# Kernel tuning notes

Measured on AMD Instinct MI355X. Metric: run time of the kernel, lower is better.

Reference implementation:

```python
import jax, jax.numpy as jnp
import numpy as np

B, N, D = 64, 256, 64          # datasets, samples per dataset, feature dim per variable (indim/2)
H, H2, OUT = 128, 64, 3        # hdlayers, hdlayers//2, outdim
REG, SIGMA, ALPHA = 1.0, 1.0, 2
BN_EPS = 1e-5


def _linear(k, fan_in, fan_out):
    kw, kb = jax.random.split(k)
    lim = 1.0 / np.sqrt(fan_in)
    w = jax.random.uniform(kw, (fan_in, fan_out), jnp.float32, -lim, lim)
    b = jax.random.uniform(kb, (fan_out,), jnp.float32, -lim, lim)
    return w, b


def setup_inputs() -> dict:
    key = jax.random.key(0)
    ks = jax.random.split(key, 10)
    w11_1, b11_1 = _linear(ks[2], D, H2)
    w11_2, b11_2 = _linear(ks[3], H2, H2)
    w12_1, b12_1 = _linear(ks[4], 2 * H2, H)
    w12_2, b12_2 = _linear(ks[5], H, H2)
    wc1, bc1 = _linear(ks[6], H2, OUT)
    w2, b2 = _linear(ks[7], OUT + 2, H2)
    wc2, bc2 = _linear(ks[8], H2, OUT)
    return {
        'x': jax.random.normal(ks[0], (B, N, D), jnp.float32),
        'y': jax.random.normal(ks[1], (B, N, D), jnp.float32),
        'w11_1': w11_1, 'b11_1': b11_1, 'w11_2': w11_2, 'b11_2': b11_2,
        'w12_1': w12_1, 'b12_1': b12_1, 'w12_2': w12_2, 'b12_2': b12_2,
        'wc1': wc1, 'bc1': bc1,
        'bn_gamma': jnp.ones((OUT + 2,), jnp.float32),
        'bn_beta': jnp.zeros((OUT + 2,), jnp.float32),
        'w2': w2, 'b2': b2, 'wc2': wc2, 'bc2': bc2,
    }


def _fro_normalize(t):
    # divide each [N, D] slice by its Frobenius norm
    return t / jnp.linalg.norm(t, axis=(1, 2), keepdims=True)


def _linear_regressor(x, y, reg):
    b, n, d = x.shape
    X = jnp.concatenate([jnp.ones((b, n, 1), x.dtype), x], axis=2)  # [B,N,d+1]
    P1 = jnp.einsum('bni,bnj->bij', X, X)                           # X^T X
    ridge = reg * jnp.eye(d + 1, dtype=x.dtype).at[0, 0].set(0.0)   # G^T G
    P2 = jnp.linalg.inv(P1 + ridge[None])
    P4 = X @ (P2 @ (jnp.swapaxes(X, 1, 2) @ y))
    loss = jnp.sum((y - P4) ** 2, axis=(1, 2))
    return loss, P4


def _gauss_kernel(x):
    # x: [B, N, F] -> [B, N, N]
    xn = jnp.sum(x * x, axis=-1)
    dist = xn[:, :, None] + xn[:, None, :] - 2.0 * jnp.einsum('bnd,bmd->bnm', x, x)
    return jnp.exp(-dist / SIGMA)


def _renyi_from_kernel(k):
    tr = jnp.trace(k, axis1=1, axis2=2)
    k = k / tr[:, None, None]
    ev = jnp.abs(jnp.linalg.eigvalsh(k))          # batched symeig eigenvalues
    return (1.0 / (1 - ALPHA)) * jnp.log2(jnp.sum(ev ** ALPHA, axis=-1))


def _renyi_mi(a, b):
    # batched normalized Renyi mutual information, a/b: [B, N, F]
    ka, kb = _gauss_kernel(a), _gauss_kernel(b)
    Hx = _renyi_from_kernel(ka)
    Hy = _renyi_from_kernel(kb)
    Hxy = _renyi_from_kernel(ka * kb)
    return (Hx + Hy - Hxy) / jnp.maximum(Hx, Hy)


def reference(x, y, w11_1, b11_1, w11_2, b11_2, w12_1, b12_1, w12_2, b12_2,
              wc1, bc1, bn_gamma, bn_beta, w2, b2, wc2, bc2):
    mlp11 = lambda t: jnp.maximum(t @ w11_1 + b11_1, 0.0) @ w11_2 + b11_2
    out_x = mlp11(x)                                  # [B,N,H2]
    out_y = mlp11(y)

    out_c = jnp.concatenate([out_x, out_y], axis=2)   # [B,N,2*H2]
    out_c = jnp.maximum(out_c @ w12_1 + b12_1, 0.0)
    out_c = jnp.maximum(out_c @ w12_2 + b12_2, 0.0)
    out_c = out_c.mean(axis=1)                        # [B,H2]
    out_c = out_c @ wc1 + bc1                         # [B,OUT]
    prob1 = jax.nn.softmax(out_c, axis=1)

    out_xn = _fro_normalize(out_x)
    out_yn = _fro_normalize(out_y)
    xx = _fro_normalize(x)
    yy = _fro_normalize(y)

    rx, px = _linear_regressor(out_xn, yy, REG)       # predict y from f(x)
    ry, py = _linear_regressor(out_yn, xx, REG)       # predict x from f(y)

    ex = _renyi_mi(yy - px, x)                        # [B]
    ey = _renyi_mi(xx - py, y)

    rxy = jnp.stack([ex, ey], axis=1)                 # [B,2]
    in_c = jnp.concatenate([out_c, rxy], axis=1)      # [B,OUT+2]
    mu = in_c.mean(axis=0)
    var = in_c.var(axis=0)                            # biased, as in torch BN training
    in_c = (in_c - mu) / jnp.sqrt(var + BN_EPS) * bn_gamma + bn_beta
    in_c = jnp.maximum(in_c @ w2 + b2, 0.0)
    out_c_f = in_c @ wc2 + bc2
    prob2 = jax.nn.softmax(out_c_f, axis=1)

    return (out_c, rx, ry, ex, ey, out_c_f, prob1, prob2)
```

## Files before the change

kernel.cpp:

```cpp
#include <hip/hip_runtime.h>
#include <math.h>

#define NB 64
#define NS 256
#define ND 64
#define NH2 64
#define NH 128
#define WSTRIDE 4224


#define F4E(v_, e_) ((e_)==0?(v_).x:((e_)==1?(v_).y:((e_)==2?(v_).z:(v_).w)))

typedef __attribute__((ext_vector_type(8))) short bf16x8;
typedef __attribute__((ext_vector_type(4))) float f32x4;

__device__ __forceinline__ unsigned short f2bf(float f){
    union { float f; unsigned int u; } v; v.f = f;
    unsigned int r = v.u + 0x7fffu + ((v.u >> 16) & 1u);
    return (unsigned short)(r >> 16);
}
__device__ __forceinline__ float bf2f(unsigned short h){
    union { unsigned int u; float f; } v; v.u = ((unsigned int)h) << 16;
    return v.f;
}
__device__ __forceinline__ void sw2(unsigned short* ph, unsigned short* pl, int idx, float f){
    unsigned short h = f2bf(f);
    ph[idx] = h;
    pl[idx] = f2bf(f - bf2f(h));
}
__device__ __forceinline__ void sw2x2(unsigned short* ph, unsigned short* pl, int idx, float f0, float f1){
    unsigned short h0 = f2bf(f0), h1 = f2bf(f1);
    ushort2 hh; hh.x = h0; hh.y = h1;
    *(ushort2*)(ph + idx) = hh;
    ushort2 ll; ll.x = f2bf(f0 - bf2f(h0)); ll.y = f2bf(f1 - bf2f(h1));
    *(ushort2*)(pl + idx) = ll;
}

#define LD8(P_, row_, kb_) (*(const bf16x8*)((const char*)(P_) + (size_t)(row_)*144 + (kb_)))

__device__ __forceinline__ f32x4 mm64(
    const unsigned short* Ah, const unsigned short* Al,
    const unsigned short* Bh, const unsigned short* Bl,
    int ar, int br, int lrow, int lkb, f32x4 acc)
{
    const int ra = ar + lrow, rb = br + lrow;
    bf16x8 ah0 = LD8(Ah, ra, lkb), ah1 = LD8(Ah, ra, lkb+64);
    bf16x8 al0 = LD8(Al, ra, lkb), al1 = LD8(Al, ra, lkb+64);
    bf16x8 bh0 = LD8(Bh, rb, lkb), bh1 = LD8(Bh, rb, lkb+64);
    bf16x8 bl0 = LD8(Bl, rb, lkb), bl1 = LD8(Bl, rb, lkb+64);
    acc = __builtin_amdgcn_mfma_f32_16x16x32_bf16(ah0, bh0, acc, 0,0,0);
    acc = __builtin_amdgcn_mfma_f32_16x16x32_bf16(ah1, bh1, acc, 0,0,0);
    acc = __builtin_amdgcn_mfma_f32_16x16x32_bf16(ah0, bl0, acc, 0,0,0);
    acc = __builtin_amdgcn_mfma_f32_16x16x32_bf16(ah1, bl1, acc, 0,0,0);
    acc = __builtin_amdgcn_mfma_f32_16x16x32_bf16(al0, bh0, acc, 0,0,0);
    acc = __builtin_amdgcn_mfma_f32_16x16x32_bf16(al1, bh1, acc, 0,0,0);
    return acc;
}

__global__ __launch_bounds__(512) void k1_fused(
    const float* __restrict__ x, const float* __restrict__ y,
    const float* __restrict__ w11_1, const float* __restrict__ b11_1,
    const float* __restrict__ w11_2, const float* __restrict__ b11_2,
    const float* __restrict__ w12_1, const float* __restrict__ b12_1,
    const float* __restrict__ w12_2, const float* __restrict__ b12_2,
    float* __restrict__ out_x, float* __restrict__ out_y,
    float* __restrict__ mean_part)
{
    const int b = blockIdx.x >> 2, tile = blockIdx.x & 3;
    const int t = threadIdx.x;
    const int lane = t & 63, wv = t >> 6;
    const int lrow = lane & 15;
    const int lkb  = (lane >> 4) * 16;
    const int row0g = b*NS + tile*64;

    __shared__ unsigned short XYh[9216], XYl[9216];
    __shared__ unsigned short W1h[4608], W1l[4608];
    __shared__ unsigned short W2h[4608], W2l[4608];
    __shared__ unsigned short Hh [9216], Hl [9216];
    __shared__ unsigned short Oh [9216], Ol [9216];
    __shared__ float msum[8*68];

    #pragma unroll
    for (int u=0;u<4;u++){
        int id = t + 512*u;
        int r = id>>4, c0 = (id&15)*4;
        const float* src = (r < 64) ? (x + ((size_t)(row0g + r))*ND)
                                    : (y + ((size_t)(row0g + r - 64))*ND);
        float4 v = *(const float4*)(src + c0);
        sw2x2(XYh, XYl, r*72 + c0,   v.x, v.y);
        sw2x2(XYh, XYl, r*72 + c0+2, v.z, v.w);
    }
    {
        int rp = t>>4, c0 = (t&15)*4;
        float4 a0 = *(const float4*)(w11_1 + (size_t)(2*rp  )*64 + c0);
        float4 a1 = *(const float4*)(w11_1 + (size_t)(2*rp+1)*64 + c0);
        float4 b0 = *(const float4*)(w11_2 + (size_t)(2*rp  )*64 + c0);
        float4 b1 = *(const float4*)(w11_2 + (size_t)(2*rp+1)*64 + c0);
        #pragma unroll
        for (int i2=0;i2<4;i2++){
            sw2x2(W1h, W1l, (c0+i2)*72 + 2*rp, F4E(a0,i2), F4E(a1,i2));
            sw2x2(W2h, W2l, (c0+i2)*72 + 2*rp, F4E(b0,i2), F4E(b1,i2));
        }
    }
    __syncthreads();

    {
        const int ar = 16*wv;
        #pragma unroll
        for (int jt=0; jt<4; jt++){
            float bb = b11_1[jt*16 + lrow];
            f32x4 acc = {bb,bb,bb,bb};
            acc = mm64(XYh, XYl, W1h, W1l, ar, jt*16, lrow, lkb, acc);
            #pragma unroll
            for (int e=0;e<4;e++){
                int row = ar + (lane>>4)*4 + e;
                int col = jt*16 + lrow;
                sw2(Hh, Hl, row*72 + col, fmaxf(acc[e], 0.f));
            }
        }
    }
    __syncthreads();

    #pragma unroll
    for (int u=0;u<2;u++){
        int id = t + 512*u;
        int krp = id>>5, c0 = (id&31)*4;
        float4 v0 = *(const float4*)(w12_1 + (size_t)(2*krp  )*NH + c0);
        float4 v1 = *(const float4*)(w12_1 + (size_t)(2*krp+1)*NH + c0);
        #pragma unroll
        for (int i2=0;i2<4;i2++)
            sw2x2(XYh, XYl, (c0+i2)*72 + 2*krp, F4E(v0,i2), F4E(v1,i2));
    }
    {
        const int ar = 16*wv;
        #pragma unroll
        for (int jt=0; jt<4; jt++){
            float bb = b11_2[jt*16 + lrow];
            f32x4 acc = {bb,bb,bb,bb};
            acc = mm64(Hh, Hl, W2h, W2l, ar, jt*16, lrow, lkb, acc);
            #pragma unroll
            for (int e=0;e<4;e++){
                int row = ar + (lane>>4)*4 + e;
                int col = jt*16 + lrow;
                float v = acc[e];
                sw2(Oh, Ol, row*72 + col, v);
                float* dst = (row < 64) ? out_x : out_y;
                dst[((size_t)(row0g + (row & 63)))*NH2 + col] = v;
            }
        }
    }
    __syncthreads();

    const int rt = wv & 3, cq = wv >> 2;
    f32x4 acc3[4];
    #pragma unroll
    for (int q=0; q<4; q++){
        float bb = b12_1[(4*cq+q)*16 + lrow];
        f32x4 v = {bb,bb,bb,bb};
        acc3[q] = v;
    }
    #pragma unroll
    for (int q=0; q<4; q++)
        acc3[q] = mm64(Oh, Ol, XYh, XYl, 16*rt, 16*(4*cq+q), lrow, lkb, acc3[q]);
    __syncthreads();

    #pragma unroll
    for (int u=0;u<2;u++){
        int id = t + 512*u;
        int krp = id>>5, c0 = (id&31)*4;
        float4 v0 = *(const float4*)(w12_1 + (size_t)(64+2*krp  )*NH + c0);
        float4 v1 = *(const float4*)(w12_1 + (size_t)(64+2*krp+1)*NH + c0);
        #pragma unroll
        for (int i2=0;i2<4;i2++)
            sw2x2(XYh, XYl, (c0+i2)*72 + 2*krp, F4E(v0,i2), F4E(v1,i2));
    }
    {
        int krp = t>>4, c0 = (t&15)*4;
        float4 h0a = *(const float4*)(w12_2 + (size_t)(2*krp  )*NH2 + c0);
        float4 h0b = *(const float4*)(w12_2 + (size_t)(2*krp+1)*NH2 + c0);
        float4 h1a = *(const float4*)(w12_2 + (size_t)(64+2*krp  )*NH2 + c0);
        float4 h1b = *(const float4*)(w12_2 + (size_t)(64+2*krp+1)*NH2 + c0);
        #pragma unroll
        for (int i2=0;i2<4;i2++){
            sw2x2(W2h, W2l, (c0+i2)*72 + 2*krp, F4E(h0a,i2), F4E(h0b,i2));
            sw2x2(W1h, W1l, (c0+i2)*72 + 2*krp, F4E(h1a,i2), F4E(h1b,i2));
        }
    }
    __syncthreads();

    #pragma unroll
    for (int q=0; q<4; q++)
        acc3[q] = mm64(Oh, Ol, XYh, XYl, 64 + 16*rt, 16*(4*cq+q), lrow, lkb, acc3[q]);
    #pragma unroll
    for (int q=0; q<4; q++){
        #pragma unroll
        for (int e=0;e<4;e++){
            int row = 16*rt + (lane>>4)*4 + e;
            int col = 16*(4*cq+q) + lrow;
            float v = fmaxf(acc3[q][e], 0.f);
            int idx = (col < 64) ? (row*72 + col) : ((64+row)*72 + (col-64));
            sw2(Hh, Hl, idx, v);
        }
    }
    __syncthreads();

    {
        f32x4 acc2[2];
        #pragma unroll
        for (int q=0; q<2; q++){
            const int jc = 2*cq + q;
            float bb = b12_2[jc*16 + lrow];
            f32x4 v = {bb,bb,bb,bb};
            acc2[q] = v;
            acc2[q] = mm64(Hh, Hl, W2h, W2l, 16*rt,      16*jc, lrow, lkb, acc2[q]);
            acc2[q] = mm64(Hh, Hl, W1h, W1l, 64 + 16*rt, 16*jc, lrow, lkb, acc2[q]);
        }
        #pragma unroll
        for (int q=0; q<2; q++){
            const int jc = 2*cq + q;
            float s = fmaxf(acc2[q][0],0.f) + fmaxf(acc2[q][1],0.f)
                    + fmaxf(acc2[q][2],0.f) + fmaxf(acc2[q][3],0.f);
            s += __shfl_down(s, 32);
            s += __shfl_down(s, 16);
            if (lane < 16) msum[wv*68 + jc*16 + lane] = s;
        }
    }
    __syncthreads();
    if (t < 64){
        const int w0 = (t>>5)*4;
        float ss = msum[(w0+0)*68 + t] + msum[(w0+1)*68 + t]
                 + msum[(w0+2)*68 + t] + msum[(w0+3)*68 + t];
        mean_part[((size_t)(b*4+tile))*64 + t] = ss;
    }
}

__global__ __launch_bounds__(256) void k2ab(
    const float* __restrict__ fx, const float* __restrict__ fy,
    const float* __restrict__ x, const float* __restrict__ y,
    float* __restrict__ wbuf)
{
    const int bs = blockIdx.x;
    const int side = bs & 1, b = bs >> 1;
    const float* feat = side ? fy : fx;
    const float* targ = side ? x : y;
    float* wb = wbuf + (size_t)bs*WSTRIDE;
    const int t = threadIdx.x;
    const int lane = t & 63, wv = t >> 6;
    const int lrow = lane & 15;
    const int lkb  = (lane >> 4) * 16;
    const float inv256 = 1.0f/256.0f;

    __shared__ float Wf[64*68];
    __shared__ float Rf[64*68];
    __shared__ unsigned short Zh[4608], Zl[4608], Th[4608], Tl[4608];
    __shared__ unsigned short Eh[4608], El[4608];
    __shared__ unsigned short Wth[2][4608], Wtl[2][4608];
    __shared__ float cspA[16*68], cspB[16*68];
    __shared__ float szs[64], sts[64];
    __shared__ float sc[8], red4[4];

    {
        float szp0=0.f,szp1=0.f,szp2=0.f,szp3=0.f;
        float stp0=0.f,stp1=0.f,stp2=0.f,stp3=0.f;
        float tsq=0.f;
        for (int c=0;c<4;c++){
            #pragma unroll
            for (int u=0;u<4;u++){
                int id = t + 256*u;
                int r = id>>4, c0 = (id&15)*4;
                float4 v = *(const float4*)(feat + ((size_t)(b*NS + c*64 + r))*NH2 + c0);
                float4 w = *(const float4*)(targ + ((size_t)(b*NS + c*64 + r))*ND + c0);
                szp0+=v.x; szp1+=v.y; szp2+=v.z; szp3+=v.w;
                stp0+=w.x; stp1+=w.y; stp2+=w.z; stp3+=w.w;
                tsq += w.x*w.x + w.y*w.y + w.z*w.z + w.w*w.w;
            }
        }
        const int g2 = t>>4, c0 = (t&15)*4;
        cspA[g2*68 + c0+0] = szp0; cspA[g2*68 + c0+1] = szp1;
        cspA[g2*68 + c0+2] = szp2; cspA[g2*68 + c0+3] = szp3;
        cspB[g2*68 + c0+0] = stp0; cspB[g2*68 + c0+1] = stp1;
        cspB[g2*68 + c0+2] = stp2; cspB[g2*68 + c0+3] = stp3;
        float tq = tsq;
        #pragma unroll
        for (int off=32; off; off>>=1) tq += __shfl_down(tq, off);
        if (lane==0) red4[wv] = tq;
    }
    __syncthreads();
    if (t < 64){
        float sa=0.f, sb=0.f;
        #pragma unroll
        for (int g2=0; g2<16; g2++){ sa += cspA[g2*68+t]; sb += cspB[g2*68+t]; }
        szs[t] = sa; sts[t] = sb;
        float s2 = sa*sa;
        #pragma unroll
        for (int off=32; off; off>>=1) s2 += __shfl_down(s2, off);
        if (t==0) sc[2] = s2;
    }
    if (t==0) sc[1] = red4[0]+red4[1]+red4[2]+red4[3];
    __syncthreads();

    f32x4 accA[4], accR[4];
    #pragma unroll
    for (int jt=0;jt<4;jt++){
        f32x4 z = {0.f,0.f,0.f,0.f};
        accA[jt]=z; accR[jt]=z;
    }
    for (int c=0;c<4;c++){
        if (c) __syncthreads();
        #pragma unroll
        for (int u=0;u<4;u++){
            int id = t + 256*u;
            int r = id>>4, c0 = (id&15)*4;
            float4 v = *(const float4*)(feat + ((size_t)(b*NS + c*64 + r))*NH2 + c0);
            float4 w = *(const float4*)(targ + ((size_t)(b*NS + c*64 + r))*ND + c0);
            v.x -= szs[c0+0]*inv256; v.y -= szs[c0+1]*inv256;
            v.z -= szs[c0+2]*inv256; v.w -= szs[c0+3]*inv256;
            sw2(Zh,Zl,(c0+0)*72+r, v.x); sw2(Zh,Zl,(c0+1)*72+r, v.y);
            sw2(Zh,Zl,(c0+2)*72+r, v.z); sw2(Zh,Zl,(c0+3)*72+r, v.w);
            sw2(Th,Tl,(c0+0)*72+r, w.x); sw2(Th,Tl,(c0+1)*72+r, w.y);
            sw2(Th,Tl,(c0+2)*72+r, w.z); sw2(Th,Tl,(c0+3)*72+r, w.w);
        }
        __syncthreads();
        #pragma unroll
        for (int jt=0;jt<4;jt++){
            accA[jt] = mm64(Zh,Zl,Zh,Zl, 16*wv, 16*jt, lrow, lkb, accA[jt]);
            accR[jt] = mm64(Zh,Zl,Th,Tl, 16*wv, 16*jt, lrow, lkb, accR[jt]);
        }
    }
    {
        const int gi0 = 16*wv + (lane>>4)*4;
        #pragma unroll
        for (int jt=0;jt<4;jt++){
            #pragma unroll
            for (int e=0;e<4;e++){
                Wf[(gi0+e)*68 + 16*jt + lrow] = accA[jt][e];
                Rf[(gi0+e)*68 + 16*jt + lrow] = accR[jt][e];
            }
        }
    }
    __syncthreads();
    if (t<64){
        float dg = Wf[t*68+t];
        #pragma unroll
        for (int off=32; off; off>>=1) dg += __shfl_down(dg, off);
        if (t==0){
            float zn2 = dg + sc[2]*inv256;
            sc[0] = 1.0f/sqrtf(zn2);
            sc[1] = 1.0f/sqrtf(sc[1]);
        }
    }
    __syncthreads();
    const float zinv = sc[0], tinv = sc[1];
    const float z2 = zinv*zinv, zt = zinv*tinv;
    const float i23 = 2.0f/3.0f, i13 = 1.0f/3.0f;
    const int i = t>>2, qd = t&3;
    {
        #pragma unroll
        for (int q=0;q<4;q++){
            const int j = qd*16 + q*4;
            float4 a4 = *(const float4*)(Wf + i*68 + j);
            float e0 = i23*z2*a4.x - ((i==j  ) ? i13 : 0.f);
            float e1 = i23*z2*a4.y - ((i==j+1) ? i13 : 0.f);
            float e2 = i23*z2*a4.z - ((i==j+2) ? i13 : 0.f);
            float e3 = i23*z2*a4.w - ((i==j+3) ? i13 : 0.f);
            sw2x2(Eh, El, i*72 + j,   e0, e1);
            sw2x2(Eh, El, i*72 + j+2, e2, e3);
            float4 rv = *(float4*)(Rf + i*68 + j);
            float r0 = i23*zt*rv.x;
            float r1 = i23*zt*rv.y;
            float r2 = i23*zt*rv.z;
            float r3 = i23*zt*rv.w;
            *(float4*)(Rf + i*68 + j) = make_float4(r0,r1,r2,r3);
            sw2(Wth[0], Wtl[0], (j  )*72 + i, r0);
            sw2(Wth[0], Wtl[0], (j+1)*72 + i, r1);
            sw2(Wth[0], Wtl[0], (j+2)*72 + i, r2);
            sw2(Wth[0], Wtl[0], (j+3)*72 + i, r3);
        }
    }
    __syncthreads();

    int cur = 0;
    for (int n=0; n<12; n++){
        f32x4 acc[4];
        #pragma unroll
        for (int jt=0; jt<4; jt++){
            f32x4 zz = {0.f,0.f,0.f,0.f};
            acc[jt] = mm64(Eh, El, Wth[cur], Wtl[cur], 16*wv, jt*16, lrow, lkb, zz);
        }
        const int gi0 = 16*wv + (lane>>4)*4;
        #pragma unroll
        for (int jt=0; jt<4; jt++){
            const int gj = jt*16 + lrow;
            float w0 = Rf[(gi0  )*68 + gj] - acc[jt][0];
            float w1 = Rf[(gi0+1)*68 + gj] - acc[jt][1];
            float w2 = Rf[(gi0+2)*68 + gj] - acc[jt][2];
            float w3 = Rf[(gi0+3)*68 + gj] - acc[jt][3];
            sw2x2(Wth[cur^1], Wtl[cur^1], gj*72 + gi0,   w0, w1);
            sw2x2(Wth[cur^1], Wtl[cur^1], gj*72 + gi0+2, w2, w3);
            if (n == 11){
                Wf[(gi0  )*68 + gj] = w0;  wb[(gi0  )*64 + gj] = w0;
                Wf[(gi0+1)*68 + gj] = w1;  wb[(gi0+1)*64 + gj] = w1;
                Wf[(gi0+2)*68 + gj] = w2;  wb[(gi0+2)*64 + gj] = w2;
                Wf[(gi0+3)*68 + gj] = w3;  wb[(gi0+3)*64 + gj] = w3;
            }
        }
        cur ^= 1;
        __syncthreads();
    }

    if (t < 64){
        float s = 0.f;
        for (int i2=0; i2<64; i2++) s += szs[i2]*Wf[i2*68 + t];
        wb[4096+t] = (tinv*sts[t] - zinv*s) * inv256;
    }
    if (t==0){ wb[4160] = zinv; wb[4161] = tinv; }
}

__global__ __launch_bounds__(256) void kRG(
    const float* __restrict__ fx, const float* __restrict__ fy,
    const float* __restrict__ x, const float* __restrict__ y,
    const float* __restrict__ wbuf,
    float* __restrict__ part3, float* __restrict__ dout)
{
    const int blk = blockIdx.x;
    const int jh = blk & 1;
    const int b = (blk >> 1) & (NB-1);
    const int side = (blk >> 1) >> 6;
    const float* feat = side ? fy : fx;
    const float* targ = side ? x : y;
    const float* bmat = side ? y : x;
    const float* wb = wbuf + (size_t)(b*2+side)*WSTRIDE;
    const int t = threadIdx.x;
    const int lane = t & 63, wv = t >> 6;
    const int lrow = lane & 15, lkb = (lane>>4)*16;

    __shared__ unsigned short resA[256*72];
    __shared__ unsigned short tgB [256*72];
    __shared__ unsigned short Zh[2*4608], Zl[2*4608];
    __shared__ unsigned short Wth[4608], Wtl[4608];
    __shared__ float c0s[64];
    __shared__ float nAs[256], nBs[256];
    __shared__ float red[4][3];
    __shared__ float lred[4];

    #pragma unroll
    for (int u=0;u<4;u++){
        int id = t + 256*u;
        int k = id>>4, c0 = (id&15)*4;
        float4 v = *(const float4*)(wb + (size_t)k*64 + c0);
        sw2(Wth, Wtl, (c0+0)*72 + k, v.x);
        sw2(Wth, Wtl, (c0+1)*72 + k, v.y);
        sw2(Wth, Wtl, (c0+2)*72 + k, v.z);
        sw2(Wth, Wtl, (c0+3)*72 + k, v.w);
    }
    if (t<64) c0s[t] = wb[4096+t];
    const float zinv = wb[4160], tinv = wb[4161];
    #pragma unroll
    for (int u=0;u<16;u++){
        int id = t + 256*u;
        int r = id>>4, c0 = (id&15)*4;
        float4 v = *(const float4*)(bmat + ((size_t)(b*NS+r))*ND + c0);
        ushort4 h;
        h.x=f2bf(v.x); h.y=f2bf(v.y); h.z=f2bf(v.z); h.w=f2bf(v.w);
        *(ushort4*)(tgB + r*72 + c0) = h;
    }
    #pragma unroll
    for (int u=0;u<4;u++){
        int id = t + 256*u;
        int r = id>>4, c0 = (id&15)*4;
        float4 v = *(const float4*)(feat + ((size_t)(b*NS + r))*NH2 + c0);
        sw2x2(Zh, Zl, r*72+c0,   v.x, v.y);
        sw2x2(Zh, Zl, r*72+c0+2, v.z, v.w);
    }
    __syncthreads();

    float lacc = 0.f;
    for (int c=0; c<4; c++){
        if (c < 3){
            unsigned short* zh = Zh + ((c+1)&1)*4608;
            unsigned short* zl = Zl + ((c+1)&1)*4608;
            #pragma unroll
            for (int u=0;u<4;u++){
                int id = t + 256*u;
                int r = id>>4, c0 = (id&15)*4;
                float4 v = *(const float4*)(feat + ((size_t)(b*NS + (c+1)*64 + r))*NH2 + c0);
                sw2x2(zh, zl, r*72+c0,   v.x, v.y);
                sw2x2(zh, zl, r*72+c0+2, v.z, v.w);
            }
        }
        const unsigned short* zh = Zh + (c&1)*4608;
        const unsigned short* zl = Zl + (c&1)*4608;
        f32x4 acc[4];
        #pragma unroll
        for (int jt=0; jt<4; jt++){
            f32x4 zz = {0.f,0.f,0.f,0.f};
            acc[jt] = mm64(zh, zl, Wth, Wtl, 16*wv, jt*16, lrow, lkb, zz);
        }
        const int r0 = 16*wv + (lane>>4)*4;
        #pragma unroll
        for (int jt=0; jt<4; jt++){
            const int gj = jt*16 + lrow;
            const float cc = c0s[gj];
            #pragma unroll
            for (int e=0;e<4;e++){
                const int grow = c*64 + r0 + e;
                float q = targ[((size_t)(b*NS+grow))*ND + gj];
                float rr = tinv*q - zinv*acc[jt][e] - cc;
                lacc += rr*rr;
                resA[grow*72 + gj] = f2bf(rr);
            }
        }
        __syncthreads();
    }

    {
        float l = lacc;
        #pragma unroll
        for (int off=32; off; off>>=1) l += __shfl_down(l, off);
        if (lane==0) lred[wv] = l;
    }
    {
        float sa=0.f, sb=0.f;
        #pragma unroll
        for (int j8=0;j8<8;j8++){
            bf16x8 va = *(const bf16x8*)((const char*)resA + (size_t)t*144 + j8*16);
            bf16x8 vb = *(const bf16x8*)((const char*)tgB  + (size_t)t*144 + j8*16);
            #pragma unroll
            for (int e2=0;e2<8;e2++){
                float fa = bf2f((unsigned short)va[e2]);
                float fb = bf2f((unsigned short)vb[e2]);
                sa += fa*fa; sb += fb*fb;
            }
        }
        nAs[t] = sa; nBs[t] = sb;
    }
    __syncthreads();
    if (t==0 && jh==0)
        dout[(side?256:192)+b] = lred[0]+lred[1]+lred[2]+lred[3];

    const char* pA = (const char*)resA;
    const char* pB = (const char*)tgB;
    const f32x4 zero4 = {0.f, 0.f, 0.f, 0.f};
    const float CEXP = -2.8853900817779268f;

    float Sa=0.f, Sb=0.f, Sab=0.f;
    #pragma unroll
    for (int it=0; it<4; it++){
        const int i0 = wv*64 + it*16;
        const int arow = i0 + lrow;
        bf16x8 aA0 = *(const bf16x8*)(pA + arow*144 + lkb);
        bf16x8 aA1 = *(const bf16x8*)(pA + arow*144 + lkb + 64);
        bf16x8 aB0 = *(const bf16x8*)(pB + arow*144 + lkb);
        bf16x8 aB1 = *(const bf16x8*)(pB + arow*144 + lkb + 64);
        float nAi[4], nBi[4];
        #pragma unroll
        for (int e=0;e<4;e++){
            int gi = i0 + (lane>>4)*4 + e;
            nAi[e] = nAs[gi]; nBi[e] = nBs[gi];
        }
        #pragma unroll
        for (int jt=0; jt<8; jt++){
            const int j0 = jh*128 + jt*16;
            const int brow = j0 + lrow;
            bf16x8 bA0 = *(const bf16x8*)(pA + brow*144 + lkb);
            bf16x8 bA1 = *(const bf16x8*)(pA + brow*144 + lkb + 64);
            bf16x8 bB0 = *(const bf16x8*)(pB + brow*144 + lkb);
            bf16x8 bB1 = *(const bf16x8*)(pB + brow*144 + lkb + 64);
            f32x4 cA = __builtin_amdgcn_mfma_f32_16x16x32_bf16(aA0, bA0, zero4, 0, 0, 0);
            cA = __builtin_amdgcn_mfma_f32_16x16x32_bf16(aA1, bA1, cA, 0, 0, 0);
            f32x4 cB = __builtin_amdgcn_mfma_f32_16x16x32_bf16(aB0, bB0, zero4, 0, 0, 0);
            cB = __builtin_amdgcn_mfma_f32_16x16x32_bf16(aB1, bB1, cB, 0, 0, 0);
            const int gj = j0 + lrow;
            const float nAj = nAs[gj], nBj = nBs[gj];
            #pragma unroll
            for (int e=0;e<4;e++){
                const int gi = i0 + (lane>>4)*4 + e;
                const float dda = (gi==gj) ? 0.f : (nAi[e] + nAj - 2.f*cA[e]);
                const float ddb = (gi==gj) ? 0.f : (nBi[e] + nBj - 2.f*cB[e]);
                const float ka2 = exp2f(CEXP*dda);
                const float kb2 = exp2f(CEXP*ddb);
                Sa += ka2; Sb += kb2; Sab += ka2*kb2;
            }
        }
    }
    #pragma unroll
    for (int off=32; off; off>>=1){
        Sa += __shfl_down(Sa,off); Sb += __shfl_down(Sb,off); Sab += __shfl_down(Sab,off);
    }
    if (lane==0){ red[wv][0]=Sa; red[wv][1]=Sb; red[wv][2]=Sab; }
    __syncthreads();
    if (t==0){
        float* o = part3 + (size_t)blk*3;
        o[0] = red[0][0]+red[1][0]+red[2][0]+red[3][0];
        o[1] = red[0][1]+red[1][1]+red[2][1]+red[3][1];
        o[2] = red[0][2]+red[1][2]+red[2][2]+red[3][2];
    }
}

__global__ __launch_bounds__(64) void k4_final(
    const float* __restrict__ mean_part, const float* __restrict__ part3,
    const float* __restrict__ wc1, const float* __restrict__ bc1,
    const float* __restrict__ bn_gamma, const float* __restrict__ bn_beta,
    const float* __restrict__ w2, const float* __restrict__ b2,
    const float* __restrict__ wc2, const float* __restrict__ bc2,
    float* __restrict__ dout)
{
    const int t = threadIdx.x;
    __shared__ float ic[64][5];
    __shared__ float mu[5], iv[5];

    float o0 = bc1[0], o1 = bc1[1], o2 = bc1[2];
    for (int c=0;c<64;c++){
        float mv = mean_part[(t*4+0)*64+c] + mean_part[(t*4+1)*64+c]
                 + mean_part[(t*4+2)*64+c] + mean_part[(t*4+3)*64+c];
        mv *= (1.0f/256.0f);
        o0 += mv*wc1[c*3+0]; o1 += mv*wc1[c*3+1]; o2 += mv*wc1[c*3+2];
    }
    dout[t*3+0]=o0; dout[t*3+1]=o1; dout[t*3+2]=o2;
    {
        float m = fmaxf(o0,fmaxf(o1,o2));
        float e0=__expf(o0-m), e1=__expf(o1-m), e2=__expf(o2-m);
        float inv = 1.f/(e0+e1+e2);
        dout[640+t*3+0]=e0*inv; dout[640+t*3+1]=e1*inv; dout[640+t*3+2]=e2*inv;
    }
    float exy[2];
    #pragma unroll
    for (int side=0; side<2; side++){
        const float* pp = part3 + (size_t)((side*NB + t)*2)*3;
        float Sa = pp[0]+pp[3];
        float Sb = pp[1]+pp[4];
        float Sab= pp[2]+pp[5];
        float Hx  = 16.f - log2f(Sa);
        float Hy  = 16.f - log2f(Sb);
        float Hxy = 16.f - log2f(Sab);
        float mi = (Hx + Hy - Hxy) / fmaxf(Hx, Hy);
        dout[(side?384:320)+t] = mi;
        exy[side] = mi;
    }
    ic[t][0]=o0; ic[t][1]=o1; ic[t][2]=o2; ic[t][3]=exy[0]; ic[t][4]=exy[1];
    __syncthreads();
    if (t<5){
        float m=0.f;
        for (int bb=0;bb<64;bb++) m += ic[bb][t];
        m *= (1.f/64.f);
        float v=0.f;
        for (int bb=0;bb<64;bb++){ float d=ic[bb][t]-m; v+=d*d; }
        v *= (1.f/64.f);
        mu[t]=m; iv[t]=1.f/sqrtf(v+1e-5f);
    }
    __syncthreads();
    float vn[5];
    #pragma unroll
    for (int c=0;c<5;c++) vn[c] = (ic[t][c]-mu[c])*iv[c]*bn_gamma[c]+bn_beta[c];
    float q0=bc2[0], q1=bc2[1], q2=bc2[2];
    for (int j=0;j<64;j++){
        float hh = b2[j];
        #pragma unroll
        for (int c=0;c<5;c++) hh += vn[c]*w2[c*64+j];
        hh = fmaxf(hh,0.f);
        q0 += hh*wc2[j*3+0]; q1 += hh*wc2[j*3+1]; q2 += hh*wc2[j*3+2];
    }
    dout[448+t*3+0]=q0; dout[448+t*3+1]=q1; dout[448+t*3+2]=q2;
    float m = fmaxf(q0,fmaxf(q1,q2));
    float e0=__expf(q0-m), e1=__expf(q1-m), e2=__expf(q2-m);
    float inv=1.f/(e0+e1+e2);
    dout[832+t*3+0]=e0*inv; dout[832+t*3+1]=e1*inv; dout[832+t*3+2]=e2*inv;
}

extern "C" void kernel_launch(void* const* d_in, const int* in_sizes, int n_in,
                              void* d_out, int out_size, void* d_ws, size_t ws_size,
                              hipStream_t stream)
{
    const float* x     = (const float*)d_in[0];
    const float* y     = (const float*)d_in[1];
    const float* w11_1 = (const float*)d_in[2];
    const float* b11_1 = (const float*)d_in[3];
    const float* w11_2 = (const float*)d_in[4];
    const float* b11_2 = (const float*)d_in[5];
    const float* w12_1 = (const float*)d_in[6];
    const float* b12_1 = (const float*)d_in[7];
    const float* w12_2 = (const float*)d_in[8];
    const float* b12_2 = (const float*)d_in[9];
    const float* wc1   = (const float*)d_in[10];
    const float* bc1   = (const float*)d_in[11];
    const float* bn_g  = (const float*)d_in[12];
    const float* bn_b  = (const float*)d_in[13];
    const float* w2    = (const float*)d_in[14];
    const float* b2    = (const float*)d_in[15];
    const float* wc2   = (const float*)d_in[16];
    const float* bc2   = (const float*)d_in[17];

    float* ws   = (float*)d_ws;
    float* dout = (float*)d_out;
    float* out_x = ws;
    float* out_y = ws + 1048576;
    float* mean_part = ws + 2097152;
    float* part3 = mean_part + 16384;
    float* wbuf  = part3 + 3840;

    hipLaunchKernelGGL(k1_fused, dim3(NB*4), dim3(512), 0, stream,
        x,y,w11_1,b11_1,w11_2,b11_2,w12_1,b12_1,w12_2,b12_2,
        out_x,out_y,mean_part);
    hipLaunchKernelGGL(k2ab, dim3(2*NB), dim3(256), 0, stream,
        out_x,out_y,x,y,wbuf);
    hipLaunchKernelGGL(kRG, dim3(NB*2*2), dim3(256), 0, stream,
        out_x,out_y,x,y,wbuf,part3,dout);
    hipLaunchKernelGGL(k4_final, dim3(1), dim3(64), 0, stream,
        mean_part,part3,wc1,bc1,bn_g,bn_b,w2,b2,wc2,bc2,dout);
}
```

Measured before the change: 79.80 us.

## Double kRG block size to 512 threads and split work across 8 waves

Raises the kRG workgroup from 256 to 512 threads. Each wave now handles half the output columns in the regression MFMA stage and half the row tiles in the Gaussian-kernel pairwise stage, and the staging loops and reductions are adjusted to 8 waves. With only 256 blocks in the grid, the aim is more waves per CU, giving better latency hiding and shorter per-block critical paths. The cost is more register pressure under the 512 launch bound and some idle threads in the norm computation.

```diff
diff --git a/kernel.cpp b/kernel.cpp
--- a/kernel.cpp
+++ b/kernel.cpp
@@ -416,7 +416,7 @@
     if (t==0){ wb[4160] = zinv; wb[4161] = tinv; }
 }
 
-__global__ __launch_bounds__(256) void kRG(
+__global__ __launch_bounds__(512) void kRG(
     const float* __restrict__ fx, const float* __restrict__ fy,
     const float* __restrict__ x, const float* __restrict__ y,
     const float* __restrict__ wbuf,
@@ -440,12 +440,12 @@
     __shared__ unsigned short Wth[4608], Wtl[4608];
     __shared__ float c0s[64];
     __shared__ float nAs[256], nBs[256];
-    __shared__ float red[4][3];
-    __shared__ float lred[4];
-
-    #pragma unroll
-    for (int u=0;u<4;u++){
-        int id = t + 256*u;
+    __shared__ float red[8][3];
+    __shared__ float lred[8];
+
+    #pragma unroll
+    for (int u=0;u<2;u++){
+        int id = t + 512*u;
         int k = id>>4, c0 = (id&15)*4;
         float4 v = *(const float4*)(wb + (size_t)k*64 + c0);
         sw2(Wth, Wtl, (c0+0)*72 + k, v.x);
@@ -456,8 +456,8 @@
     if (t<64) c0s[t] = wb[4096+t];
     const float zinv = wb[4160], tinv = wb[4161];
     #pragma unroll
-    for (int u=0;u<16;u++){
-        int id = t + 256*u;
+    for (int u=0;u<8;u++){
+        int id = t + 512*u;
         int r = id>>4, c0 = (id&15)*4;
         float4 v = *(const float4*)(bmat + ((size_t)(b*NS+r))*ND + c0);
         ushort4 h;
@@ -465,8 +465,8 @@
         *(ushort4*)(tgB + r*72 + c0) = h;
     }
     #pragma unroll
-    for (int u=0;u<4;u++){
-        int id = t + 256*u;
+    for (int u=0;u<2;u++){
+        int id = t + 512*u;
         int r = id>>4, c0 = (id&15)*4;
         float4 v = *(const float4*)(feat + ((size_t)(b*NS + r))*NH2 + c0);
         sw2x2(Zh, Zl, r*72+c0,   v.x, v.y);
@@ -474,14 +474,15 @@
     }
     __syncthreads();
 
+    const int rt = wv & 3, cq = wv >> 2;
     float lacc = 0.f;
     for (int c=0; c<4; c++){
         if (c < 3){
             unsigned short* zh = Zh + ((c+1)&1)*4608;
             unsigned short* zl = Zl + ((c+1)&1)*4608;
             #pragma unroll
-            for (int u=0;u<4;u++){
-                int id = t + 256*u;
+            for (int u=0;u<2;u++){
+                int id = t + 512*u;
                 int r = id>>4, c0 = (id&15)*4;
                 float4 v = *(const float4*)(feat + ((size_t)(b*NS + (c+1)*64 + r))*NH2 + c0);
                 sw2x2(zh, zl, r*72+c0,   v.x, v.y);
@@ -490,22 +491,22 @@
         }
         const unsigned short* zh = Zh + (c&1)*4608;
         const unsigned short* zl = Zl + (c&1)*4608;
-        f32x4 acc[4];
-        #pragma unroll
-        for (int jt=0; jt<4; jt++){
+        f32x4 acc[2];
+        #pragma unroll
+        for (int q=0; q<2; q++){
             f32x4 zz = {0.f,0.f,0.f,0.f};
-            acc[jt] = mm64(zh, zl, Wth, Wtl, 16*wv, jt*16, lrow, lkb, zz);
-        }
-        const int r0 = 16*wv + (lane>>4)*4;
-        #pragma unroll
-        for (int jt=0; jt<4; jt++){
-            const int gj = jt*16 + lrow;
+            acc[q] = mm64(zh, zl, Wth, Wtl, 16*rt, 16*(2*cq+q), lrow, lkb, zz);
+        }
+        const int r0 = 16*rt + (lane>>4)*4;
+        #pragma unroll
+        for (int q=0; q<2; q++){
+            const int gj = 16*(2*cq+q) + lrow;
             const float cc = c0s[gj];
             #pragma unroll
             for (int e=0;e<4;e++){
                 const int grow = c*64 + r0 + e;
-                float q = targ[((size_t)(b*NS+grow))*ND + gj];
-                float rr = tinv*q - zinv*acc[jt][e] - cc;
+                float qv = targ[((size_t)(b*NS+grow))*ND + gj];
+                float rr = tinv*qv - zinv*acc[q][e] - cc;
                 lacc += rr*rr;
                 resA[grow*72 + gj] = f2bf(rr);
             }
@@ -519,7 +520,7 @@
         for (int off=32; off; off>>=1) l += __shfl_down(l, off);
         if (lane==0) lred[wv] = l;
     }
-    {
+    if (t < 256){
         float sa=0.f, sb=0.f;
         #pragma unroll
         for (int j8=0;j8<8;j8++){
@@ -535,8 +536,12 @@
         nAs[t] = sa; nBs[t] = sb;
     }
     __syncthreads();
-    if (t==0 && jh==0)
-        dout[(side?256:192)+b] = lred[0]+lred[1]+lred[2]+lred[3];
+    if (t==0 && jh==0){
+        float ls = 0.f;
+        #pragma unroll
+        for (int w=0;w<8;w++) ls += lred[w];
+        dout[(side?256:192)+b] = ls;
+    }
 
     const char* pA = (const char*)resA;
     const char* pB = (const char*)tgB;
@@ -545,8 +550,8 @@
 
     float Sa=0.f, Sb=0.f, Sab=0.f;
     #pragma unroll
-    for (int it=0; it<4; it++){
-        const int i0 = wv*64 + it*16;
+    for (int it=0; it<2; it++){
+        const int i0 = wv*32 + it*16;
         const int arow = i0 + lrow;
         bf16x8 aA0 = *(const bf16x8*)(pA + arow*144 + lkb);
         bf16x8 aA1 = *(const bf16x8*)(pA + arow*144 + lkb + 64);
@@ -590,10 +595,11 @@
     if (lane==0){ red[wv][0]=Sa; red[wv][1]=Sb; red[wv][2]=Sab; }
     __syncthreads();
     if (t==0){
+        float s0=0.f, s1=0.f, s2=0.f;
+        #pragma unroll
+        for (int w=0;w<8;w++){ s0 += red[w][0]; s1 += red[w][1]; s2 += red[w][2]; }
         float* o = part3 + (size_t)blk*3;
-        o[0] = red[0][0]+red[1][0]+red[2][0]+red[3][0];
-        o[1] = red[0][1]+red[1][1]+red[2][1]+red[3][1];
-        o[2] = red[0][2]+red[1][2]+red[2][2]+red[3][2];
+        o[0] = s0; o[1] = s1; o[2] = s2;
     }
 }
 
@@ -703,7 +709,7 @@
         out_x,out_y,mean_part);
     hipLaunchKernelGGL(k2ab, dim3(2*NB), dim3(256), 0, stream,
         out_x,out_y,x,y,wbuf);
-    hipLaunchKernelGGL(kRG, dim3(NB*2*2), dim3(256), 0, stream,
+    hipLaunchKernelGGL(kRG, dim3(NB*2*2), dim3(512), 0, stream,
         out_x,out_y,x,y,wbuf,part3,dout);
     hipLaunchKernelGGL(k4_final, dim3(1), dim3(64), 0, stream,
         mean_part,part3,wc1,bc1,bn_g,bn_b,w2,b2,wc2,bc2,dout);
```

Result: faster. 77.17 us (-3.3%).
